# Performance work log

Measured on AMD Instinct MI355X. Metric: run time of the kernel, lower is better.

Reference implementation:

```python
import jax, jax.numpy as jnp
import numpy as np

D, M, ALPHA = 64, 512, 7.18
DIM = 1024
B = M * D  # batch: M clusters x D samples each


def setup_inputs() -> dict:
    key = jax.random.key(0)
    outputs = jax.random.normal(key, (B, DIM), dtype=jnp.float32)
    indices = jnp.arange(B, dtype=jnp.int64 if jax.config.jax_enable_x64 else jnp.int32)
    assignment = indices // D  # sample i -> cluster i//D (contiguous blocks of D)
    loss_vector = jnp.zeros((M,), jnp.float32)
    loss_count = jnp.zeros((M,), jnp.float32)
    return {"outputs": outputs, "indices": indices, "assignment": assignment,
            "loss_vector": loss_vector, "loss_count": loss_count}


def reference(outputs, indices, assignment, loss_vector, loss_count):
    outputs = outputs.astype(jnp.float32)
    own = assignment[indices]                              # [B] cluster id per sample
    n = jnp.float32(B)
    # cluster means (each cluster has exactly D samples)
    means = jax.ops.segment_sum(outputs, own, num_segments=M) / D   # [M, DIM]
    # pooled variance: sum ||x_i - mu_{c(i)}||^2 / (N - 1)
    diff_own = outputs - means[own]
    var_sum = jnp.sum(diff_own * diff_own)
    stdev = -2.0 * var_sum / (n - 1.0)                     # the (negative) -2*sigma^2 term
    # squared distances to every cluster mean: [B, M]
    sq = (jnp.sum(outputs * outputs, axis=1)[:, None]
          + jnp.sum(means * means, axis=1)[None, :]
          - 2.0 * outputs @ means.T)
    exps = jnp.exp(sq / stdev)                             # [B, M]
    own_col = own[:, None]
    own_exp = jnp.take_along_axis(exps, own_col, axis=1)[:, 0]
    denom = jnp.sum(exps, axis=1) - own_exp                # sum over mF != own
    sq_own = jnp.take_along_axis(sq, own_col, axis=1)[:, 0]
    log_ratio = sq_own / stdev - ALPHA - jnp.log(denom)    # log(exp(.-alpha)/denom)
    per_loss = jnp.maximum(-log_ratio, 0.0)                # == -clamp(log_ratio, max=0)
    loss = (jnp.sum(per_loss) / n).reshape(1)
    lv = (loss_vector + jax.ops.segment_sum(per_loss, own, num_segments=M)) / n
    lc = loss_count + jax.ops.segment_sum(jnp.ones((B,), jnp.float32), own, num_segments=M)
    variance = var_sum / (n - 1.0)                         # stdev / -2.0 in the original
    return loss, lv, lc, variance
```

## Files before the change

### kernel.cpp

```cpp
#include <hip/hip_runtime.h>
#include <hip/hip_bf16.h>
#include <stdint.h>

#define DIM 1024
#define ALPHA 7.18f
#define INV_N (1.0f/32768.0f)
#define NM1 32767.0f
#define LOG2E 1.44269504088896f
#define LN2 0.693147180559945f

typedef __attribute__((ext_vector_type(8))) short bfrag8;
typedef __attribute__((ext_vector_type(4))) float f32x4;

typedef const __attribute__((address_space(1))) void gv_t;
typedef __attribute__((address_space(3))) void lv_t;

__device__ __forceinline__ unsigned f2bf_bits(float f) {
    unsigned u = __float_as_uint(f);
    return (u + 0x7fffu + ((u >> 16) & 1u)) >> 16;
}

__global__ __launch_bounds__(512)
void k1_colsum(const float* __restrict__ outputs, const int* __restrict__ indices,
               const int* __restrict__ assignment, float* __restrict__ mean_sums,
               unsigned* __restrict__ counts, float* __restrict__ scalars,
               int* __restrict__ own_g) {
    __shared__ int sown[64];
    __shared__ int suni;
    __shared__ float4 spart[8][64];
    __shared__ float ssq[8];
    const int tid = threadIdx.x;
    const int rg = blockIdx.x >> 2, cq = blockIdx.x & 3;
    const int row0 = rg * 64;
    if (tid == 0) suni = 1;
    if (tid < 64) {
        int m = assignment[indices[row0 + tid]];
        sown[tid] = m;
        if (cq == 0) { own_g[row0 + tid] = m; atomicAdd(&counts[m], 1u); }
    }
    __syncthreads();
    if (tid < 63 && sown[tid] != sown[tid + 1]) suni = 0;
    __syncthreads();

    const int c4 = tid & 63;
    const int rq = tid >> 6;
    const float* gp = outputs + (size_t)(row0 + rq * 8) * DIM + cq * 256 + c4 * 4;
    float4 s4 = {0.f, 0.f, 0.f, 0.f};
    float sq = 0.f;

    if (suni) {
        float4 v[8];
        #pragma unroll
        for (int r = 0; r < 8; ++r) v[r] = *(const float4*)(gp + (size_t)r * DIM);
        #pragma unroll
        for (int r = 0; r < 8; ++r) {
            sq = fmaf(v[r].x, v[r].x, sq); sq = fmaf(v[r].y, v[r].y, sq);
            sq = fmaf(v[r].z, v[r].z, sq); sq = fmaf(v[r].w, v[r].w, sq);
            s4.x += v[r].x; s4.y += v[r].y; s4.z += v[r].z; s4.w += v[r].w;
        }
        spart[rq][c4] = s4;
        __syncthreads();
        if (rq == 0) {
            #pragma unroll
            for (int r = 1; r < 8; ++r) {
                float4 o = spart[r][c4];
                s4.x += o.x; s4.y += o.y; s4.z += o.z; s4.w += o.w;
            }
            float* dst = mean_sums + (size_t)sown[0] * DIM + cq * 256 + c4 * 4;
            atomicAdd(dst + 0, s4.x); atomicAdd(dst + 1, s4.y);
            atomicAdd(dst + 2, s4.z); atomicAdd(dst + 3, s4.w);
        }
    } else {
        int curm = sown[rq * 8];
        for (int r = 0; r < 8; ++r) {
            float4 v = *(const float4*)(gp + (size_t)r * DIM);
            int m = sown[rq * 8 + r];
            if (m != curm) {
                float* dst = mean_sums + (size_t)curm * DIM + cq * 256 + c4 * 4;
                atomicAdd(dst + 0, s4.x); atomicAdd(dst + 1, s4.y);
                atomicAdd(dst + 2, s4.z); atomicAdd(dst + 3, s4.w);
                s4 = (float4){0.f, 0.f, 0.f, 0.f};
                curm = m;
            }
            sq = fmaf(v.x, v.x, sq); sq = fmaf(v.y, v.y, sq);
            sq = fmaf(v.z, v.z, sq); sq = fmaf(v.w, v.w, sq);
            s4.x += v.x; s4.y += v.y; s4.z += v.z; s4.w += v.w;
        }
        float* dst = mean_sums + (size_t)curm * DIM + cq * 256 + c4 * 4;
        atomicAdd(dst + 0, s4.x); atomicAdd(dst + 1, s4.y);
        atomicAdd(dst + 2, s4.z); atomicAdd(dst + 3, s4.w);
        __syncthreads();
    }

    #pragma unroll
    for (int mk = 32; mk; mk >>= 1) sq += __shfl_xor(sq, mk, 64);
    if ((tid & 63) == 0) ssq[tid >> 6] = sq;
    __syncthreads();
    if (tid == 0) {
        float s = 0.f;
        #pragma unroll
        for (int w = 0; w < 8; ++w) s += ssq[w];
        atomicAdd(&scalars[0], s);
    }
}

__global__ __launch_bounds__(256)
void k2_means(const float* __restrict__ mean_sums, const unsigned* __restrict__ counts,
              unsigned short* __restrict__ b_kt, float* __restrict__ msq,
              float* __restrict__ scalars) {
    const int m = blockIdx.x, t = threadIdx.x;
    const float* row = mean_sums + (size_t)m * DIM;
    float4 v = *(const float4*)(row + t * 4);
    float4 mu = {v.x * (1.0f/64.0f), v.y * (1.0f/64.0f), v.z * (1.0f/64.0f), v.w * (1.0f/64.0f)};
    const int tt = t >> 3, kc = (t >> 1) & 3, half = t & 1;
    unsigned lo = f2bf_bits(mu.x) | (f2bf_bits(mu.y) << 16);
    unsigned hi = f2bf_bits(mu.z) | (f2bf_bits(mu.w) << 16);
    *(uint2*)((char*)b_kt + tt * 32768 + m * 64 + ((kc ^ ((m >> 1) & 3)) << 4) + half * 8)
        = make_uint2(lo, hi);
    float sq = fmaf(mu.x, mu.x, fmaf(mu.y, mu.y, fmaf(mu.z, mu.z, mu.w * mu.w)));
    #pragma unroll
    for (int mk = 32; mk; mk >>= 1) sq += __shfl_xor(sq, mk, 64);
    __shared__ float sw[4];
    if ((t & 63) == 0) sw[t >> 6] = sq;
    __syncthreads();
    if (t == 0) {
        float s = sw[0] + sw[1] + sw[2] + sw[3];
        msq[m] = s;
        atomicAdd(&scalars[1], ((float)counts[m] - 128.0f) * s);
    }
}

__global__ __launch_bounds__(512)
void k3_finalize(float* __restrict__ scalars, const float* __restrict__ msq,
                 const unsigned* __restrict__ counts, const float* __restrict__ loss_vector,
                 const float* __restrict__ loss_count, float* __restrict__ msl,
                 float* __restrict__ out) {
    const int t = threadIdx.x;
    float var_sum = scalars[0] + scalars[1];
    float inv_std = -NM1 / (2.0f * var_sum);
    msl[t] = msq[t] * inv_std * LOG2E;
    out[1 + t] = loss_vector[t] * INV_N;
    out[513 + t] = loss_count[t] + (float)counts[t];
    if (t == 0) {
        out[0] = 0.0f;
        out[1025] = var_sum / NM1;
        scalars[2] = inv_std;
    }
}

__global__ __launch_bounds__(512)
void k4_gemm(const float* __restrict__ outputs, const unsigned short* __restrict__ b_kt,
             const float* __restrict__ msl, const float* __restrict__ scalars,
             const int* __restrict__ own_g, float* __restrict__ out) {
    __shared__ short lA[2][64 * 32];
    __shared__ short lB[2][512 * 32];
    __shared__ float red_sum[64][4];
    __shared__ float red_own[64][4];

    const int tid  = threadIdx.x;
    const int lane = tid & 63;
    const int wid  = tid >> 6;
    const int wm   = wid >> 2;
    const int wn   = wid & 3;
    const int brow = blockIdx.x * 64;

    const int rA = tid >> 3;
    const int kq = tid & 7;
    const float* gA = outputs + (size_t)(brow + rA) * DIM + kq * 4;
    const int aw_byte = rA * 64 + (((kq >> 1) ^ ((rA >> 1) & 3)) << 4) + ((kq & 1) << 3);

    const int arow = wm * 32 + (lane & 15);
    const int ar_byte = arow * 64 + (((lane >> 4) ^ ((arow >> 1) & 3)) << 4);
    const int bcol = wn * 128 + (lane & 15);
    const int br_byte = bcol * 64 + (((lane >> 4) ^ ((bcol >> 1) & 3)) << 4);

    const char* bbase = (const char*)b_kt;

    f32x4 acc[2][8];
    #pragma unroll
    for (int i = 0; i < 2; ++i)
        #pragma unroll
        for (int j = 0; j < 8; ++j)
            acc[i][j] = (f32x4){0.f, 0.f, 0.f, 0.f};

    #pragma unroll
    for (int i = 0; i < 4; ++i) {
        const char* gsrc = bbase + (wid * 4 + i) * 1024 + lane * 16;
        char* ldst = (char*)&lB[0][0] + (wid * 4 + i) * 1024;
        __builtin_amdgcn_global_load_lds((gv_t*)gsrc, (lv_t*)ldst, 16, 0, 0);
    }
    {
        float4 areg = *(const float4*)gA;
        unsigned lo = f2bf_bits(areg.x) | (f2bf_bits(areg.y) << 16);
        unsigned hi = f2bf_bits(areg.z) | (f2bf_bits(areg.w) << 16);
        *(uint2*)((char*)&lA[0][0] + aw_byte) = make_uint2(lo, hi);
    }
    __syncthreads();

    int cur = 0;
    for (int t = 0; t < 32; ++t) {
        const bool has_next = (t + 1) < 32;
        float4 anext;
        if (has_next) {
            anext = *(const float4*)(gA + (t + 1) * 32);
            #pragma unroll
            for (int i = 0; i < 4; ++i) {
                const char* gsrc = bbase + (size_t)(t + 1) * 32768 + (wid * 4 + i) * 1024 + lane * 16;
                char* ldst = (char*)&lB[cur ^ 1][0] + (wid * 4 + i) * 1024;
                __builtin_amdgcn_global_load_lds((gv_t*)gsrc, (lv_t*)ldst, 16, 0, 0);
            }
        }

        const char* pa = (const char*)&lA[cur][0] + ar_byte;
        const char* pb = (const char*)&lB[cur][0] + br_byte;
        bfrag8 a0 = *(const bfrag8*)(pa);
        bfrag8 a1 = *(const bfrag8*)(pa + 1024);
        #pragma unroll
        for (int fn = 0; fn < 8; ++fn) {
            bfrag8 bf = *(const bfrag8*)(pb + fn * 1024);
            acc[0][fn] = __builtin_amdgcn_mfma_f32_16x16x32_bf16(a0, bf, acc[0][fn], 0, 0, 0);
            acc[1][fn] = __builtin_amdgcn_mfma_f32_16x16x32_bf16(a1, bf, acc[1][fn], 0, 0, 0);
        }

        if (has_next) {
            unsigned lo = f2bf_bits(anext.x) | (f2bf_bits(anext.y) << 16);
            unsigned hi = f2bf_bits(anext.z) | (f2bf_bits(anext.w) << 16);
            *(uint2*)((char*)&lA[cur ^ 1][0] + aw_byte) = make_uint2(lo, hi);
        }
        __syncthreads();
        cur ^= 1;
    }

    float mslv[8];
    #pragma unroll
    for (int fn = 0; fn < 8; ++fn) mslv[fn] = msl[bcol + fn * 16];
    const float inv_std = scalars[2];
    const float c2k = -2.0f * inv_std * LOG2E;
    int ownv[2][4];
    #pragma unroll
    for (int fm = 0; fm < 2; ++fm)
        #pragma unroll
        for (int rg = 0; rg < 4; ++rg)
            ownv[fm][rg] = own_g[brow + wm * 32 + fm * 16 + ((lane >> 4) << 2) + rg];

    #pragma unroll
    for (int fm = 0; fm < 2; ++fm) {
        #pragma unroll
        for (int rg = 0; rg < 4; ++rg) {
            float sum = 0.f, oa = -1e30f;
            int ownr = ownv[fm][rg];
            #pragma unroll
            for (int fn = 0; fn < 8; ++fn) {
                float dot = acc[fm][fn][rg];
                float arg = fmaf(c2k, dot, mslv[fn]);
                sum += exp2f(arg);
                bool isown = (bcol + fn * 16) == ownr;
                oa = isown ? arg : oa;
            }
            #pragma unroll
            for (int mk = 1; mk < 16; mk <<= 1) {
                sum += __shfl_xor(sum, mk, 64);
                oa = fmaxf(oa, __shfl_xor(oa, mk, 64));
            }
            if ((lane & 15) == 0) {
                int r_in = wm * 32 + fm * 16 + ((lane >> 4) << 2) + rg;
                red_sum[r_in][wn] = sum;
                red_own[r_in][wn] = oa;
            }
        }
    }
    __syncthreads();

    if (tid < 64) {
        float s = red_sum[tid][0] + red_sum[tid][1] + red_sum[tid][2] + red_sum[tid][3];
        float oa = fmaxf(fmaxf(red_own[tid][0], red_own[tid][1]),
                         fmaxf(red_own[tid][2], red_own[tid][3]));
        float denom = s - exp2f(oa);
        float per_loss = fmaxf(ALPHA + LN2 * (log2f(denom) - oa), 0.f);
        int ownr = own_g[brow + tid];
        float ls = per_loss;
        #pragma unroll
        for (int mk = 1; mk < 64; mk <<= 1) ls += __shfl_xor(ls, mk, 64);
        int own0 = __shfl(ownr, 0, 64);
        if (__all(ownr == own0)) {
            if (tid == 0) atomicAdd(&out[1 + own0], ls * INV_N);
        } else {
            atomicAdd(&out[1 + ownr], per_loss * INV_N);
        }
        if (tid == 0) atomicAdd(&out[0], ls * INV_N);
    }
}

extern "C" void kernel_launch(void* const* d_in, const int* in_sizes, int n_in,
                              void* d_out, int out_size, void* d_ws, size_t ws_size,
                              hipStream_t stream) {
    const float* outputs     = (const float*)d_in[0];
    const int*   indices     = (const int*)d_in[1];
    const int*   assignment  = (const int*)d_in[2];
    const float* loss_vector = (const float*)d_in[3];
    const float* loss_count  = (const float*)d_in[4];
    float* out = (float*)d_out;

    char* ws = (char*)d_ws;
    float*          mean_sums = (float*)ws;
    unsigned*       counts    = (unsigned*)(ws + 2097152);
    float*          scalars   = (float*)(ws + 2099200);
    const size_t    ZB        = 2099456;
    unsigned short* b_kt      = (unsigned short*)(ws + 2101248);
    float*          msq       = (float*)(ws + 3149824);
    float*          msl       = (float*)(ws + 3151872);
    int*            own_g     = (int*)(ws + 3153920);

    hipMemsetAsync(d_ws, 0, ZB, stream);
    hipLaunchKernelGGL(k1_colsum, dim3(2048), dim3(512), 0, stream,
                       outputs, indices, assignment, mean_sums, counts, scalars, own_g);
    hipLaunchKernelGGL(k2_means, dim3(512), dim3(256), 0, stream,
                       mean_sums, counts, b_kt, msq, scalars);
    hipLaunchKernelGGL(k3_finalize, dim3(1), dim3(512), 0, stream,
                       scalars, msq, counts, loss_vector, loss_count, msl, out);
    hipLaunchKernelGGL(k4_gemm, dim3(512), dim3(512), 0, stream,
                       outputs, b_kt, msl, scalars, own_g, out);
}
```

Before: 330.6 us.

## Pre-convert activations to swizzled bf16 in colsum pass, triple-buffer GEMM loads

The column-sum kernel now handles 64 full rows per block and also writes the activations as bf16 in the GEMM's swizzled LDS tile layout to a workspace buffer. The GEMM kernel then loads A tiles straight into LDS with global_load_lds instead of reading fp32 and converting in registers. It also moves to a three-stage LDS ring with explicit waitcnt and barriers. This halves the GEMM's A-read bandwidth and takes the conversion off the GEMM critical path, but adds a 64 MB bf16 write in k1, reduces k1's grid to 512 blocks, and uses more LDS in k4.

```diff
diff --git a/kernel.cpp b/kernel.cpp
--- a/kernel.cpp
+++ b/kernel.cpp
@@ -24,59 +24,67 @@
 void k1_colsum(const float* __restrict__ outputs, const int* __restrict__ indices,
                const int* __restrict__ assignment, float* __restrict__ mean_sums,
                unsigned* __restrict__ counts, float* __restrict__ scalars,
-               int* __restrict__ own_g) {
+               int* __restrict__ own_g, unsigned short* __restrict__ a_bf) {
     __shared__ int sown[64];
     __shared__ int suni;
-    __shared__ float4 spart[8][64];
+    __shared__ float4 spart[256];
     __shared__ float ssq[8];
     const int tid = threadIdx.x;
-    const int rg = blockIdx.x >> 2, cq = blockIdx.x & 3;
-    const int row0 = rg * 64;
+    const int blk = blockIdx.x;
+    const int row0 = blk * 64;
     if (tid == 0) suni = 1;
     if (tid < 64) {
         int m = assignment[indices[row0 + tid]];
         sown[tid] = m;
-        if (cq == 0) { own_g[row0 + tid] = m; atomicAdd(&counts[m], 1u); }
+        own_g[row0 + tid] = m;
+        atomicAdd(&counts[m], 1u);
     }
     __syncthreads();
     if (tid < 63 && sown[tid] != sown[tid + 1]) suni = 0;
     __syncthreads();
 
-    const int c4 = tid & 63;
-    const int rq = tid >> 6;
-    const float* gp = outputs + (size_t)(row0 + rq * 8) * DIM + cq * 256 + c4 * 4;
+    const int c4 = tid & 255, rh = tid >> 8;
+    const float* gp = outputs + (size_t)(row0 + rh) * DIM + c4 * 4;
+    const int kc = (c4 >> 1) & 3, half = c4 & 1;
+    char* abase = (char*)a_bf + (size_t)blk * 131072 + (c4 >> 3) * 4096 + half * 8;
+
     float4 s4 = {0.f, 0.f, 0.f, 0.f};
     float sq = 0.f;
 
     if (suni) {
-        float4 v[8];
-        #pragma unroll
-        for (int r = 0; r < 8; ++r) v[r] = *(const float4*)(gp + (size_t)r * DIM);
-        #pragma unroll
-        for (int r = 0; r < 8; ++r) {
-            sq = fmaf(v[r].x, v[r].x, sq); sq = fmaf(v[r].y, v[r].y, sq);
-            sq = fmaf(v[r].z, v[r].z, sq); sq = fmaf(v[r].w, v[r].w, sq);
-            s4.x += v[r].x; s4.y += v[r].y; s4.z += v[r].z; s4.w += v[r].w;
-        }
-        spart[rq][c4] = s4;
+        #pragma unroll 1
+        for (int sb = 0; sb < 8; ++sb) {
+            float4 v[4];
+            #pragma unroll
+            for (int r = 0; r < 4; ++r)
+                v[r] = *(const float4*)(gp + (size_t)(sb * 8 + r * 2) * DIM);
+            #pragma unroll
+            for (int r = 0; r < 4; ++r) {
+                sq = fmaf(v[r].x, v[r].x, sq); sq = fmaf(v[r].y, v[r].y, sq);
+                sq = fmaf(v[r].z, v[r].z, sq); sq = fmaf(v[r].w, v[r].w, sq);
+                s4.x += v[r].x; s4.y += v[r].y; s4.z += v[r].z; s4.w += v[r].w;
+                int rr = sb * 8 + r * 2 + rh;
+                unsigned lo = f2bf_bits(v[r].x) | (f2bf_bits(v[r].y) << 16);
+                unsigned hi = f2bf_bits(v[r].z) | (f2bf_bits(v[r].w) << 16);
+                *(uint2*)(abase + rr * 64 + ((kc ^ ((rr >> 1) & 3)) << 4)) = make_uint2(lo, hi);
+            }
+        }
+        if (rh) spart[c4] = s4;
         __syncthreads();
-        if (rq == 0) {
-            #pragma unroll
-            for (int r = 1; r < 8; ++r) {
-                float4 o = spart[r][c4];
-                s4.x += o.x; s4.y += o.y; s4.z += o.z; s4.w += o.w;
-            }
-            float* dst = mean_sums + (size_t)sown[0] * DIM + cq * 256 + c4 * 4;
-            atomicAdd(dst + 0, s4.x); atomicAdd(dst + 1, s4.y);
-            atomicAdd(dst + 2, s4.z); atomicAdd(dst + 3, s4.w);
+        if (!rh) {
+            float4 o = spart[c4];
+            float* dst = mean_sums + (size_t)sown[0] * DIM + c4 * 4;
+            atomicAdd(dst + 0, s4.x + o.x); atomicAdd(dst + 1, s4.y + o.y);
+            atomicAdd(dst + 2, s4.z + o.z); atomicAdd(dst + 3, s4.w + o.w);
         }
     } else {
-        int curm = sown[rq * 8];
-        for (int r = 0; r < 8; ++r) {
-            float4 v = *(const float4*)(gp + (size_t)r * DIM);
-            int m = sown[rq * 8 + r];
+        int curm = sown[rh];
+        for (int r = 0; r < 32; ++r) {
+            int rr = r * 2 + rh;
+            float4 v = *(const float4*)(gp + (size_t)(r * 2) * DIM);
+            int m = sown[rr];
             if (m != curm) {
-                float* dst = mean_sums + (size_t)curm * DIM + cq * 256 + c4 * 4;
+                float* dst = mean_sums + (size_t)curm * DIM + c4 * 4;
                 atomicAdd(dst + 0, s4.x); atomicAdd(dst + 1, s4.y);
                 atomicAdd(dst + 2, s4.z); atomicAdd(dst + 3, s4.w);
                 s4 = (float4){0.f, 0.f, 0.f, 0.f};
@@ -85,8 +93,11 @@
             sq = fmaf(v.x, v.x, sq); sq = fmaf(v.y, v.y, sq);
             sq = fmaf(v.z, v.z, sq); sq = fmaf(v.w, v.w, sq);
             s4.x += v.x; s4.y += v.y; s4.z += v.z; s4.w += v.w;
-        }
-        float* dst = mean_sums + (size_t)curm * DIM + cq * 256 + c4 * 4;
+            unsigned lo = f2bf_bits(v.x) | (f2bf_bits(v.y) << 16);
+            unsigned hi = f2bf_bits(v.z) | (f2bf_bits(v.w) << 16);
+            *(uint2*)(abase + rr * 64 + ((kc ^ ((rr >> 1) & 3)) << 4)) = make_uint2(lo, hi);
+        }
+        float* dst = mean_sums + (size_t)curm * DIM + c4 * 4;
         atomicAdd(dst + 0, s4.x); atomicAdd(dst + 1, s4.y);
         atomicAdd(dst + 2, s4.z); atomicAdd(dst + 3, s4.w);
         __syncthreads();
@@ -148,12 +159,37 @@
     }
 }
 
+#define K4_STAGE(s, lab, lbb) do {                                             \
+    const char* _gb = bbase + (size_t)(s) * 32768 + (wid * 4) * 1024 + lane * 16; \
+    _Pragma("unroll")                                                          \
+    for (int _i = 0; _i < 4; ++_i)                                             \
+        __builtin_amdgcn_global_load_lds((gv_t*)(_gb + _i * 1024),             \
+                                         (lv_t*)((lbb) + (wid * 4 + _i) * 1024), 16, 0, 0); \
+    if (wid < 4) {                                                             \
+        const char* _ga = aprime + (size_t)(s) * 4096 + wid * 1024 + lane * 16; \
+        __builtin_amdgcn_global_load_lds((gv_t*)_ga, (lv_t*)((lab) + wid * 1024), 16, 0, 0); \
+    }                                                                          \
+} while (0)
+
+#define K4_COMPUTE(lab, lbb) do {                                              \
+    const char* pa = (lab) + ar_byte;                                          \
+    const char* pb = (lbb) + br_byte;                                          \
+    bfrag8 a0 = *(const bfrag8*)(pa);                                          \
+    bfrag8 a1 = *(const bfrag8*)(pa + 1024);                                   \
+    _Pragma("unroll")                                                          \
+    for (int fn = 0; fn < 8; ++fn) {                                           \
+        bfrag8 bf = *(const bfrag8*)(pb + fn * 1024);                          \
+        acc[0][fn] = __builtin_amdgcn_mfma_f32_16x16x32_bf16(a0, bf, acc[0][fn], 0, 0, 0); \
+        acc[1][fn] = __builtin_amdgcn_mfma_f32_16x16x32_bf16(a1, bf, acc[1][fn], 0, 0, 0); \
+    }                                                                          \
+} while (0)
+
 __global__ __launch_bounds__(512)
-void k4_gemm(const float* __restrict__ outputs, const unsigned short* __restrict__ b_kt,
+void k4_gemm(const unsigned short* __restrict__ a_bf, const unsigned short* __restrict__ b_kt,
              const float* __restrict__ msl, const float* __restrict__ scalars,
              const int* __restrict__ own_g, float* __restrict__ out) {
-    __shared__ short lA[2][64 * 32];
-    __shared__ short lB[2][512 * 32];
+    __shared__ short lA[3][64 * 32];
+    __shared__ short lB[3][512 * 32];
     __shared__ float red_sum[64][4];
     __shared__ float red_own[64][4];
 
@@ -164,17 +200,13 @@
     const int wn   = wid & 3;
     const int brow = blockIdx.x * 64;
 
-    const int rA = tid >> 3;
-    const int kq = tid & 7;
-    const float* gA = outputs + (size_t)(brow + rA) * DIM + kq * 4;
-    const int aw_byte = rA * 64 + (((kq >> 1) ^ ((rA >> 1) & 3)) << 4) + ((kq & 1) << 3);
-
     const int arow = wm * 32 + (lane & 15);
     const int ar_byte = arow * 64 + (((lane >> 4) ^ ((arow >> 1) & 3)) << 4);
     const int bcol = wn * 128 + (lane & 15);
     const int br_byte = bcol * 64 + (((lane >> 4) ^ ((bcol >> 1) & 3)) << 4);
 
-    const char* bbase = (const char*)b_kt;
+    const char* aprime = (const char*)a_bf + (size_t)blockIdx.x * 131072;
+    const char* bbase  = (const char*)b_kt;
 
     f32x4 acc[2][8];
     #pragma unroll
@@ -183,53 +215,29 @@
         for (int j = 0; j < 8; ++j)
             acc[i][j] = (f32x4){0.f, 0.f, 0.f, 0.f};
 
-    #pragma unroll
-    for (int i = 0; i < 4; ++i) {
-        const char* gsrc = bbase + (wid * 4 + i) * 1024 + lane * 16;
-        char* ldst = (char*)&lB[0][0] + (wid * 4 + i) * 1024;
-        __builtin_amdgcn_global_load_lds((gv_t*)gsrc, (lv_t*)ldst, 16, 0, 0);
-    }
-    {
-        float4 areg = *(const float4*)gA;
-        unsigned lo = f2bf_bits(areg.x) | (f2bf_bits(areg.y) << 16);
-        unsigned hi = f2bf_bits(areg.z) | (f2bf_bits(areg.w) << 16);
-        *(uint2*)((char*)&lA[0][0] + aw_byte) = make_uint2(lo, hi);
-    }
-    __syncthreads();
-
-    int cur = 0;
-    for (int t = 0; t < 32; ++t) {
-        const bool has_next = (t + 1) < 32;
-        float4 anext;
-        if (has_next) {
-            anext = *(const float4*)(gA + (t + 1) * 32);
-            #pragma unroll
-            for (int i = 0; i < 4; ++i) {
-                const char* gsrc = bbase + (size_t)(t + 1) * 32768 + (wid * 4 + i) * 1024 + lane * 16;
-                char* ldst = (char*)&lB[cur ^ 1][0] + (wid * 4 + i) * 1024;
-                __builtin_amdgcn_global_load_lds((gv_t*)gsrc, (lv_t*)ldst, 16, 0, 0);
-            }
-        }
-
-        const char* pa = (const char*)&lA[cur][0] + ar_byte;
-        const char* pb = (const char*)&lB[cur][0] + br_byte;
-        bfrag8 a0 = *(const bfrag8*)(pa);
-        bfrag8 a1 = *(const bfrag8*)(pa + 1024);
-        #pragma unroll
-        for (int fn = 0; fn < 8; ++fn) {
-            bfrag8 bf = *(const bfrag8*)(pb + fn * 1024);
-            acc[0][fn] = __builtin_amdgcn_mfma_f32_16x16x32_bf16(a0, bf, acc[0][fn], 0, 0, 0);
-            acc[1][fn] = __builtin_amdgcn_mfma_f32_16x16x32_bf16(a1, bf, acc[1][fn], 0, 0, 0);
-        }
-
-        if (has_next) {
-            unsigned lo = f2bf_bits(anext.x) | (f2bf_bits(anext.y) << 16);
-            unsigned hi = f2bf_bits(anext.z) | (f2bf_bits(anext.w) << 16);
-            *(uint2*)((char*)&lA[cur ^ 1][0] + aw_byte) = make_uint2(lo, hi);
-        }
-        __syncthreads();
-        cur ^= 1;
-    }
+    char* la0 = (char*)&lA[0][0]; char* la1 = (char*)&lA[1][0]; char* la2 = (char*)&lA[2][0];
+    char* lb0 = (char*)&lB[0][0]; char* lb1 = (char*)&lB[1][0]; char* lb2 = (char*)&lB[2][0];
+
+    K4_STAGE(0, la0, lb0);
+    K4_STAGE(1, la1, lb1);
+
+    #pragma unroll 1
+    for (int t = 0; t < 31; ++t) {
+        if (wid < 4) asm volatile("s_waitcnt vmcnt(5) lgkmcnt(0)" ::: "memory");
+        else         asm volatile("s_waitcnt vmcnt(4) lgkmcnt(0)" ::: "memory");
+        __builtin_amdgcn_sched_barrier(0);
+        __builtin_amdgcn_s_barrier();
+        __builtin_amdgcn_sched_barrier(0);
+        K4_COMPUTE(la0, lb0);
+        if (t < 30) K4_STAGE(t + 2, la2, lb2);
+        char* ta = la0; la0 = la1; la1 = la2; la2 = ta;
+        char* tb = lb0; lb0 = lb1; lb1 = lb2; lb2 = tb;
+    }
+    asm volatile("s_waitcnt vmcnt(0) lgkmcnt(0)" ::: "memory");
+    __builtin_amdgcn_sched_barrier(0);
+    __builtin_amdgcn_s_barrier();
+    __builtin_amdgcn_sched_barrier(0);
+    K4_COMPUTE(la0, lb0);
 
     float mslv[8];
     #pragma unroll
@@ -310,14 +318,15 @@
     float*          msq       = (float*)(ws + 3149824);
     float*          msl       = (float*)(ws + 3151872);
     int*            own_g     = (int*)(ws + 3153920);
+    unsigned short* a_bf      = (unsigned short*)(ws + 4194304);
 
     hipMemsetAsync(d_ws, 0, ZB, stream);
-    hipLaunchKernelGGL(k1_colsum, dim3(2048), dim3(512), 0, stream,
-                       outputs, indices, assignment, mean_sums, counts, scalars, own_g);
+    hipLaunchKernelGGL(k1_colsum, dim3(512), dim3(512), 0, stream,
+                       outputs, indices, assignment, mean_sums, counts, scalars, own_g, a_bf);
     hipLaunchKernelGGL(k2_means, dim3(512), dim3(256), 0, stream,
                        mean_sums, counts, b_kt, msq, scalars);
     hipLaunchKernelGGL(k3_finalize, dim3(1), dim3(512), 0, stream,
                        scalars, msq, counts, loss_vector, loss_count, msl, out);
     hipLaunchKernelGGL(k4_gemm, dim3(512), dim3(512), 0, stream,
-                       outputs, b_kt, msl, scalars, own_g, out);
-}
+                       a_bf, b_kt, msl, scalars, own_g, out);
+}
```

Result: faster. 298.4 us (-9.7%).
